# Kernel tuning notes

Hardware: AMD Instinct MI355X
Metric: run time of the kernel (lower is better)

## Reference

```python
import jax, jax.numpy as jnp
import numpy as np

N_NODES = 50000
N_EDGES = 800000
N_FEAT = 64
HIDDEN = 64
N_GRAPHS = 64
N_CLASSES = 10
BN_EPS = 1e-5


def setup_inputs() -> dict:
    key = jax.random.key(0)
    ks = jax.random.split(key, 12)
    x = jax.random.normal(ks[0], (N_NODES, N_FEAT), dtype=jnp.float32)
    edge_index = jax.random.randint(ks[1], (2, N_EDGES), 0, N_NODES, dtype=jnp.int64)
    # equal-sized, sorted graph assignment so every graph is non-empty for max-pool
    batch = (jnp.arange(N_NODES, dtype=jnp.int64) * N_GRAPHS) // N_NODES
    s = 0.1
    return {
        "x": x,
        "edge_index": edge_index,
        "batch": batch,
        "W1": jax.random.normal(ks[2], (N_FEAT, HIDDEN), jnp.float32) * s,
        "b1": jnp.zeros((HIDDEN,), jnp.float32),
        "W2": jax.random.normal(ks[3], (HIDDEN, HIDDEN), jnp.float32) * s,
        "b2": jnp.zeros((HIDDEN,), jnp.float32),
        "W3": jax.random.normal(ks[4], (HIDDEN, HIDDEN), jnp.float32) * s,
        "b3": jnp.zeros((HIDDEN,), jnp.float32),
        # NOTE: source uses [Norm(hidden)]*3 -> ONE shared BatchNorm across layers
        "gamma": jnp.ones((HIDDEN,), jnp.float32),
        "beta": jnp.zeros((HIDDEN,), jnp.float32),
        "lin1_w": jax.random.normal(ks[5], (HIDDEN, HIDDEN), jnp.float32) * s,
        "lin1_b": jnp.zeros((HIDDEN,), jnp.float32),
        "lin2_w": jax.random.normal(ks[6], (HIDDEN, N_CLASSES), jnp.float32) * s,
        "lin2_b": jnp.zeros((N_CLASSES,), jnp.float32),
    }


def reference(x, edge_index, batch, W1, b1, W2, b2, W3, b3, gamma, beta,
              lin1_w, lin1_b, lin2_w, lin2_b):
    N = x.shape[0]
    src, dst = edge_index[0], edge_index[1]
    # GCN symmetric normalization with self-loops: deg = in-degree + 1
    deg = jax.ops.segment_sum(jnp.ones(src.shape[0], x.dtype), dst, num_segments=N) + 1.0
    dis = jax.lax.rsqrt(deg)                      # [N]
    coef = (dis[src] * dis[dst])[:, None]         # [E,1] edge norm
    self_coef = (dis * dis)[:, None]              # [N,1] self-loop norm

    def gcn_conv(h, W, b):
        h = h @ W                                  # [N,H] tiny GEMM
        agg = jax.ops.segment_sum(h[src] * coef, dst, num_segments=N)
        return agg + h * self_coef + b

    def batch_norm(h):
        mu = h.mean(axis=0)
        var = h.var(axis=0)                        # biased var, torch BN training mode
        return gamma * (h - mu) * jax.lax.rsqrt(var + BN_EPS) + beta

    out = x
    for W, b in ((W1, b1), (W2, b2), (W3, b3)):
        out = jax.nn.relu(batch_norm(gcn_conv(out, W, b)))

    emb = jax.ops.segment_max(out, batch, num_segments=N_GRAPHS)  # global_max_pool
    return jax.nn.relu(emb @ lin1_w + lin1_b) @ lin2_w + lin2_b
```

## Files before the change

kernel.cpp:

```cpp
#include <hip/hip_runtime.h>
#include <hip/hip_bf16.h>

#define N_NODES 50000
#define N_EDGES 800000
#define HID 64
#define N_GRAPHS 64
#define N_CLASSES 10
#define BN_EPS 1e-5f

typedef unsigned int uint;
typedef unsigned short ushort;

__device__ __forceinline__ float blo(uint u) { return __uint_as_float(u << 16); }
__device__ __forceinline__ float bhi(uint u) { return __uint_as_float(u & 0xffff0000u); }
__device__ __forceinline__ unsigned short f2b(float f) {
  __hip_bfloat16 h = __float2bfloat16(f);
  return *reinterpret_cast<unsigned short*>(&h);
}


__global__ void k_count_deg(const int* __restrict__ dst, int* __restrict__ deg) {
  int e = blockIdx.x * blockDim.x + threadIdx.x;
  if (e < N_EDGES) atomicAdd(&deg[__builtin_nontemporal_load(&dst[e])], 1);
}

__global__ void k_scan_block(const int* __restrict__ deg, int* __restrict__ rowp,
                             int* __restrict__ bsum, float* __restrict__ dis) {
  __shared__ int s[256];
  int tid = threadIdx.x;
  int i = blockIdx.x * 256 + tid;
  int v = (i < N_NODES) ? deg[i] : 0;
  if (i < N_NODES) dis[i] = rsqrtf((float)v + 1.0f);
  s[tid] = v;
  __syncthreads();
  for (int off = 1; off < 256; off <<= 1) {
    int t = (tid >= off) ? s[tid - off] : 0;
    __syncthreads();
    s[tid] += t;
    __syncthreads();
  }
  if (i < N_NODES) rowp[i] = s[tid] - v;
  if (tid == 255) bsum[blockIdx.x] = s[255];
}

__global__ void k_scan_partials(int* __restrict__ bsum, int nb) {
  __shared__ int s[256];
  int tid = threadIdx.x;
  int v = (tid < nb) ? bsum[tid] : 0;
  s[tid] = v;
  __syncthreads();
  for (int off = 1; off < 256; off <<= 1) {
    int t = (tid >= off) ? s[tid - off] : 0;
    __syncthreads();
    s[tid] += t;
    __syncthreads();
  }
  if (tid < nb) bsum[tid] = s[tid] - v;
}

__global__ void k_scan_finish(int* __restrict__ rowp, const int* __restrict__ bsum,
                              int* __restrict__ cursor) {
  int i = blockIdx.x * blockDim.x + threadIdx.x;
  if (i < N_NODES) {
    int v = rowp[i] + bsum[i >> 8];
    rowp[i] = v;
    cursor[i] = v;
  }
  if (i == 0) rowp[N_NODES] = N_EDGES;
}

__global__ void k_fill_edges(const int* __restrict__ ei, const float* __restrict__ dis,
                             int* __restrict__ cursor, uint* __restrict__ edata) {
  int e = blockIdx.x * blockDim.x + threadIdx.x;
  if (e < N_EDGES) {
    int s = __builtin_nontemporal_load(&ei[e]);
    int d = __builtin_nontemporal_load(&ei[N_EDGES + e]);
    int pos = atomicAdd(&cursor[d], 1);
    edata[pos] = ((uint)s << 16) | f2b(dis[s] * dis[d]);
  }
}


template <bool IN_BF16>
__global__ __launch_bounds__(256) void k_gemm(const void* __restrict__ in,
                                              const float* __restrict__ W,
                                              __hip_bfloat16* __restrict__ out,
                                              float* __restrict__ stats_zero,
                                              const float* __restrict__ stats_in,
                                              const float* __restrict__ gamma,
                                              const float* __restrict__ beta) {
  __shared__ float Al[4][64];
  int tid = threadIdx.x;
  int wid = tid >> 6, f = tid & 63;
  if (blockIdx.x == 0) {
    for (int i = tid; i < 1024; i += 256) stats_zero[i] = 0.0f;
  }
  float Wreg[64];
#pragma unroll
  for (int k = 0; k < 64; ++k) Wreg[k] = W[k * 64 + f];
  float sc = 1.f, sh = 0.f;
  if (stats_in) {
    float s = 0.f, q = 0.f;
#pragma unroll
    for (int c = 0; c < 8; ++c) {
      s += stats_in[c * 128 + f];
      q += stats_in[c * 128 + 64 + f];
    }
    float mu = s * (1.0f / N_NODES);
    float var = q * (1.0f / N_NODES) - mu * mu;
    sc = gamma[f] * rsqrtf(var + BN_EPS);
    sh = beta[f] - mu * sc;
  }
  for (int n = blockIdx.x * 4 + wid; n < N_NODES; n += gridDim.x * 4) {
    float av;
    if (IN_BF16) {
      ushort u = ((const ushort*)in)[(n << 6) + f];
      av = __uint_as_float((uint)u << 16);
    } else {
      av = ((const float*)in)[(n << 6) + f];
    }
    if (stats_in) {
      av = fmaf(av, sc, sh);
      av = av > 0.f ? av : 0.f;
    }
    Al[wid][f] = av;
    float acc = 0.f;
    const float4* arow = (const float4*)Al[wid];
#pragma unroll
    for (int k4 = 0; k4 < 16; ++k4) {
      float4 a = arow[k4];
      acc = fmaf(a.x, Wreg[k4 * 4 + 0], acc);
      acc = fmaf(a.y, Wreg[k4 * 4 + 1], acc);
      acc = fmaf(a.z, Wreg[k4 * 4 + 2], acc);
      acc = fmaf(a.w, Wreg[k4 * 4 + 3], acc);
    }
    out[(n << 6) + f] = __float2bfloat16(acc);
  }
}

__global__ __launch_bounds__(256, 4) void k_agg_node(
    const __hip_bfloat16* __restrict__ hW, const float* __restrict__ dis,
    const int* __restrict__ rowp, const uint* __restrict__ edata,
    const float* __restrict__ bias, __hip_bfloat16* __restrict__ act,
    float* __restrict__ stats) {
  __shared__ float sstat[4][2][64];
  int tid = threadIdx.x;
  int wid = tid >> 6, lane = tid & 63;
  int g = lane >> 3, l8 = lane & 7;
  int n = (blockIdx.x * 4 + wid) * 8 + g;
  const uint4* hw4 = (const uint4*)hW;
  float pre[8] = {0, 0, 0, 0, 0, 0, 0, 0};
  float sq[8] = {0, 0, 0, 0, 0, 0, 0, 0};
  if (n < N_NODES) {
    int p0 = rowp[n], p1 = rowp[n + 1];
    float acc[8] = {0, 0, 0, 0, 0, 0, 0, 0};
    for (int pb = p0; pb < p1; pb += 8) {
      uint rec = (pb + l8 < p1) ? edata[pb + l8] : 0u;
      uint e[8];
#pragma unroll
      for (int u = 0; u < 8; ++u) e[u] = __shfl(rec, (g << 3) | u, 64);
#pragma unroll
      for (int h = 0; h < 2; ++h) {
        uint4 hv[4];
#pragma unroll
        for (int u = 0; u < 4; ++u) hv[u] = hw4[(e[h * 4 + u] >> 16) * 8 + l8];
#pragma unroll
        for (int u = 0; u < 4; ++u) {
          float wv = blo(e[h * 4 + u]);
          acc[0] = fmaf(blo(hv[u].x), wv, acc[0]);
          acc[1] = fmaf(bhi(hv[u].x), wv, acc[1]);
          acc[2] = fmaf(blo(hv[u].y), wv, acc[2]);
          acc[3] = fmaf(bhi(hv[u].y), wv, acc[3]);
          acc[4] = fmaf(blo(hv[u].z), wv, acc[4]);
          acc[5] = fmaf(bhi(hv[u].z), wv, acc[5]);
          acc[6] = fmaf(blo(hv[u].w), wv, acc[6]);
          acc[7] = fmaf(bhi(hv[u].w), wv, acc[7]);
        }
      }
    }
    float dn = dis[n];
    float dn2 = dn * dn;
    uint4 hs = hw4[n * 8 + l8];
    const float4* b4 = (const float4*)bias;
    float4 bA = b4[l8 * 2], bB = b4[l8 * 2 + 1];
    pre[0] = fmaf(blo(hs.x), dn2, acc[0]) + bA.x;
    pre[1] = fmaf(bhi(hs.x), dn2, acc[1]) + bA.y;
    pre[2] = fmaf(blo(hs.y), dn2, acc[2]) + bA.z;
    pre[3] = fmaf(bhi(hs.y), dn2, acc[3]) + bA.w;
    pre[4] = fmaf(blo(hs.z), dn2, acc[4]) + bB.x;
    pre[5] = fmaf(bhi(hs.z), dn2, acc[5]) + bB.y;
    pre[6] = fmaf(blo(hs.w), dn2, acc[6]) + bB.z;
    pre[7] = fmaf(bhi(hs.w), dn2, acc[7]) + bB.w;
    uint4 st;
    st.x = (uint)f2b(pre[0]) | ((uint)f2b(pre[1]) << 16);
    st.y = (uint)f2b(pre[2]) | ((uint)f2b(pre[3]) << 16);
    st.z = (uint)f2b(pre[4]) | ((uint)f2b(pre[5]) << 16);
    st.w = (uint)f2b(pre[6]) | ((uint)f2b(pre[7]) << 16);
    ((uint4*)act)[n * 8 + l8] = st;
#pragma unroll
    for (int i = 0; i < 8; ++i) sq[i] = pre[i] * pre[i];
  }
#pragma unroll
  for (int off = 8; off < 64; off <<= 1) {
#pragma unroll
    for (int i = 0; i < 8; ++i) {
      pre[i] += __shfl_xor(pre[i], off, 64);
      sq[i] += __shfl_xor(sq[i], off, 64);
    }
  }
  if (g == 0) {
#pragma unroll
    for (int i = 0; i < 8; ++i) {
      sstat[wid][0][l8 * 8 + i] = pre[i];
      sstat[wid][1][l8 * 8 + i] = sq[i];
    }
  }
  __syncthreads();
  if (tid < 128) {
    int which = tid >> 6, f = tid & 63;
    float s = sstat[0][which][f] + sstat[1][which][f] + sstat[2][which][f] +
              sstat[3][which][f];
    atomicAdd(&stats[(blockIdx.x & 7) * 128 + which * 64 + f], s);
  }
}


__global__ __launch_bounds__(256) void k_pool(const __hip_bfloat16* __restrict__ act,
                                              const float* __restrict__ stats_in,
                                              const float* __restrict__ gamma,
                                              const float* __restrict__ beta,
                                              float* __restrict__ pooled) {
  int g = blockIdx.x;
  int tid = threadIdx.x;
  int l16 = tid & 15;
  int r = tid >> 4;
  float sc[4], sh[4];
#pragma unroll
  for (int i = 0; i < 4; ++i) {
    int f = l16 * 4 + i;
    float s = 0.f, q = 0.f;
#pragma unroll
    for (int c = 0; c < 8; ++c) {
      s += stats_in[c * 128 + f];
      q += stats_in[c * 128 + 64 + f];
    }
    float mu = s * (1.0f / N_NODES);
    float var = q * (1.0f / N_NODES) - mu * mu;
    sc[i] = gamma[f] * rsqrtf(var + BN_EPS);
    sh[i] = beta[f] - mu * sc[i];
  }
  int gs = g * N_NODES;
  int start = (gs + 63) >> 6;
  int end = (gs + N_NODES + 63) >> 6;
  float m[4] = {0.f, 0.f, 0.f, 0.f};
  const uint2* a2 = (const uint2*)act;
  for (int n = start + r; n < end; n += 16) {
    uint2 v = a2[n * 16 + l16];
    m[0] = fmaxf(m[0], fmaf(blo(v.x), sc[0], sh[0]));
    m[1] = fmaxf(m[1], fmaf(bhi(v.x), sc[1], sh[1]));
    m[2] = fmaxf(m[2], fmaf(blo(v.y), sc[2], sh[2]));
    m[3] = fmaxf(m[3], fmaf(bhi(v.y), sc[3], sh[3]));
  }
  __shared__ float sm[16][64];
#pragma unroll
  for (int i = 0; i < 4; ++i) sm[r][l16 * 4 + i] = m[i];
  __syncthreads();
  if (tid < 64) {
    float mm = sm[0][tid];
#pragma unroll
    for (int rr = 1; rr < 16; ++rr) mm = fmaxf(mm, sm[rr][tid]);
    pooled[g * 64 + tid] = mm;
  }
}

__global__ __launch_bounds__(256) void k_final(const float* __restrict__ pooled,
                                               const float* __restrict__ w1,
                                               const float* __restrict__ b1,
                                               const float* __restrict__ w2,
                                               const float* __restrict__ b2,
                                               float* __restrict__ out) {
  __shared__ float P[64 * 64];
  __shared__ float Hd[64 * 64];
  int tid = threadIdx.x;
  for (int i = tid; i < 4096; i += 256) P[i] = pooled[i];
  __syncthreads();
  for (int i = tid; i < 4096; i += 256) {
    int g = i >> 6, j = i & 63;
    float acc = b1[j];
#pragma unroll
    for (int k = 0; k < 64; ++k) acc = fmaf(P[g * 64 + k], w1[k * 64 + j], acc);
    Hd[i] = acc > 0.f ? acc : 0.f;
  }
  __syncthreads();
  for (int i = tid; i < 640; i += 256) {
    int g = i / 10, c = i % 10;
    float acc = b2[c];
#pragma unroll
    for (int k = 0; k < 64; ++k) acc = fmaf(Hd[g * 64 + k], w2[k * 10 + c], acc);
    out[i] = acc;
  }
}


extern "C" void kernel_launch(void* const* d_in, const int* in_sizes, int n_in,
                              void* d_out, int out_size, void* d_ws, size_t ws_size,
                              hipStream_t stream) {
  const float* x = (const float*)d_in[0];
  const int* ei = (const int*)d_in[1];
  const float* W1 = (const float*)d_in[3];
  const float* b1 = (const float*)d_in[4];
  const float* W2 = (const float*)d_in[5];
  const float* b2 = (const float*)d_in[6];
  const float* W3 = (const float*)d_in[7];
  const float* b3 = (const float*)d_in[8];
  const float* gamma = (const float*)d_in[9];
  const float* beta = (const float*)d_in[10];
  const float* l1w = (const float*)d_in[11];
  const float* l1b = (const float*)d_in[12];
  const float* l2w = (const float*)d_in[13];
  const float* l2b = (const float*)d_in[14];
  float* out = (float*)d_out;

  char* ws = (char*)d_ws;
  size_t off = 0;
  auto alloc = [&](size_t bytes) {
    void* p = ws + off;
    off = (off + bytes + 255) & ~(size_t)255;
    return p;
  };
  int* deg = (int*)alloc(N_NODES * 4);
  int* rowp = (int*)alloc((N_NODES + 1) * 4);
  int* cursor = (int*)alloc(N_NODES * 4);
  int* bsum = (int*)alloc(256 * 4);
  uint* edata = (uint*)alloc((size_t)N_EDGES * 4);
  float* dis = (float*)alloc(N_NODES * 4);
  __hip_bfloat16* hW = (__hip_bfloat16*)alloc((size_t)N_NODES * 64 * 2);
  __hip_bfloat16* act = (__hip_bfloat16*)alloc((size_t)N_NODES * 64 * 2);
  float* statsL0 = (float*)alloc(1024 * 4);
  float* statsL1 = (float*)alloc(1024 * 4);
  float* statsL2 = (float*)alloc(1024 * 4);
  float* pooled = (float*)alloc(4096 * 4);

  int nsb = (N_NODES + 255) / 256;
  int nag = (N_NODES + 31) / 32;

  (void)hipMemsetAsync(deg, 0, N_NODES * 4, stream);
  k_count_deg<<<(N_EDGES + 255) / 256, 256, 0, stream>>>(ei + N_EDGES, deg);
  k_scan_block<<<nsb, 256, 0, stream>>>(deg, rowp, bsum, dis);
  k_scan_partials<<<1, 256, 0, stream>>>(bsum, nsb);
  k_scan_finish<<<nsb, 256, 0, stream>>>(rowp, bsum, cursor);
  k_fill_edges<<<(N_EDGES + 255) / 256, 256, 0, stream>>>(ei, dis, cursor, edata);

  k_gemm<false><<<2048, 256, 0, stream>>>(x, W1, hW, statsL0, nullptr, gamma, beta);
  k_agg_node<<<nag, 256, 0, stream>>>(hW, dis, rowp, edata, b1, act, statsL0);
  k_gemm<true><<<2048, 256, 0, stream>>>(act, W2, hW, statsL1, statsL0, gamma, beta);
  k_agg_node<<<nag, 256, 0, stream>>>(hW, dis, rowp, edata, b2, act, statsL1);
  k_gemm<true><<<2048, 256, 0, stream>>>(act, W3, hW, statsL2, statsL1, gamma, beta);
  k_agg_node<<<nag, 256, 0, stream>>>(hW, dis, rowp, edata, b3, act, statsL2);

  k_pool<<<N_GRAPHS, 256, 0, stream>>>(act, statsL2, gamma, beta, pooled);
  k_final<<<1, 256, 0, stream>>>(pooled, l1w, l1b, l2w, l2b, out);
}
```

Measured before the change: 230.1 us.

## Build CSR with two-pass bucketed partition instead of global atomic scatter

```diff
diff --git a/kernel.cpp b/kernel.cpp
--- a/kernel.cpp
+++ b/kernel.cpp
@@ -7,6 +7,8 @@
 #define N_GRAPHS 64
 #define N_CLASSES 10
 #define BN_EPS 1e-5f
+#define NPART 196
+#define FILL_BLOCKS 128
 
 typedef unsigned int uint;
 typedef unsigned short ushort;
@@ -59,24 +61,69 @@
 }
 
 __global__ void k_scan_finish(int* __restrict__ rowp, const int* __restrict__ bsum,
-                              int* __restrict__ cursor) {
+                              int* __restrict__ pcur) {
   int i = blockIdx.x * blockDim.x + threadIdx.x;
   if (i < N_NODES) {
     int v = rowp[i] + bsum[i >> 8];
     rowp[i] = v;
-    cursor[i] = v;
+    if ((i & 255) == 0) pcur[i >> 8] = v;
   }
   if (i == 0) rowp[N_NODES] = N_EDGES;
 }
 
-__global__ void k_fill_edges(const int* __restrict__ ei, const float* __restrict__ dis,
-                             int* __restrict__ cursor, uint* __restrict__ edata) {
-  int e = blockIdx.x * blockDim.x + threadIdx.x;
-  if (e < N_EDGES) {
+__global__ __launch_bounds__(256) void k_partA(const int* __restrict__ ei,
+                                               int* __restrict__ pcur,
+                                               uint* __restrict__ tmp) {
+  __shared__ int lcnt[NPART];
+  __shared__ int lbase[NPART];
+  int tid = threadIdx.x;
+  const int per = (N_EDGES + FILL_BLOCKS - 1) / FILL_BLOCKS;
+  int c0 = blockIdx.x * per;
+  int c1 = c0 + per;
+  if (c1 > N_EDGES) c1 = N_EDGES;
+  for (int i = tid; i < NPART; i += 256) lcnt[i] = 0;
+  __syncthreads();
+  for (int e = c0 + tid; e < c1; e += 256) {
+    int d = __builtin_nontemporal_load(&ei[N_EDGES + e]);
+    atomicAdd(&lcnt[d >> 8], 1);
+  }
+  __syncthreads();
+  for (int p = tid; p < NPART; p += 256) lbase[p] = atomicAdd(&pcur[p], lcnt[p]);
+  __syncthreads();
+  for (int e = c0 + tid; e < c1; e += 256) {
     int s = __builtin_nontemporal_load(&ei[e]);
     int d = __builtin_nontemporal_load(&ei[N_EDGES + e]);
-    int pos = atomicAdd(&cursor[d], 1);
-    edata[pos] = ((uint)s << 16) | f2b(dis[s] * dis[d]);
+    int pos = atomicAdd(&lbase[d >> 8], 1);
+    tmp[pos] = ((uint)s << 8) | (uint)(d & 255);
+  }
+}
+
+__global__ __launch_bounds__(256) void k_partB(const uint* __restrict__ tmp,
+                                               const int* __restrict__ rowp,
+                                               const float* __restrict__ dis,
+                                               uint* __restrict__ edata) {
+  __shared__ int cur[256];
+  __shared__ float sdis[256];
+  int tid = threadIdx.x;
+  int p = blockIdx.x;
+  int n0 = p << 8;
+  {
+    int n = n0 + tid;
+    cur[tid] = (n < N_NODES) ? rowp[n] : 0;
+    sdis[tid] = (n < N_NODES) ? dis[n] : 0.f;
+  }
+  int base = rowp[n0];
+  int endn = n0 + 256;
+  if (endn > N_NODES) endn = N_NODES;
+  int pend = rowp[endn];
+  __syncthreads();
+  for (int idx = base + tid; idx < pend; idx += 256) {
+    uint t = __builtin_nontemporal_load(&tmp[idx]);
+    uint s = t >> 8;
+    uint dl = t & 255u;
+    int pos = atomicAdd(&cur[dl], 1);
+    float coef = dis[s] * sdis[dl];
+    edata[pos] = (s << 16) | (uint)f2b(coef);
   }
 }
 
@@ -330,8 +377,9 @@
   };
   int* deg = (int*)alloc(N_NODES * 4);
   int* rowp = (int*)alloc((N_NODES + 1) * 4);
-  int* cursor = (int*)alloc(N_NODES * 4);
+  int* pcur = (int*)alloc(NPART * 4);
   int* bsum = (int*)alloc(256 * 4);
+  uint* tmp = (uint*)alloc((size_t)N_EDGES * 4);
   uint* edata = (uint*)alloc((size_t)N_EDGES * 4);
   float* dis = (float*)alloc(N_NODES * 4);
   __hip_bfloat16* hW = (__hip_bfloat16*)alloc((size_t)N_NODES * 64 * 2);
@@ -348,8 +396,9 @@
   k_count_deg<<<(N_EDGES + 255) / 256, 256, 0, stream>>>(ei + N_EDGES, deg);
   k_scan_block<<<nsb, 256, 0, stream>>>(deg, rowp, bsum, dis);
   k_scan_partials<<<1, 256, 0, stream>>>(bsum, nsb);
-  k_scan_finish<<<nsb, 256, 0, stream>>>(rowp, bsum, cursor);
-  k_fill_edges<<<(N_EDGES + 255) / 256, 256, 0, stream>>>(ei, dis, cursor, edata);
+  k_scan_finish<<<nsb, 256, 0, stream>>>(rowp, bsum, pcur);
+  k_partA<<<FILL_BLOCKS, 256, 0, stream>>>(ei, pcur, tmp);
+  k_partB<<<NPART, 256, 0, stream>>>(tmp, rowp, dis, edata);
 
   k_gemm<false><<<2048, 256, 0, stream>>>(x, W1, hW, statsL0, nullptr, gamma, beta);
   k_agg_node<<<nag, 256, 0, stream>>>(hW, dis, rowp, edata, b1, act, statsL0);
```

After: 227.0 us. About the same (-1.4%).
